# Kernel tuning notes

Hardware: AMD Instinct MI355X
Metric: run time of the kernel (lower is better)

## Reference

```python
import jax, jax.numpy as jnp
import numpy as np

N_NODES = 100000
IN_DIM = 64
OUT_DIM = 64
N_EDGES = 1600000


def _undirected_self_loops(edge_index, num_nodes):
    """Symmetrize, add self loops, coalesce (dedup+sort) like the torch module.
    edge_index is an integer constant, so we preprocess with numpy (no grads flow here).
    Returns (src, dst, w) where w are symmetric GCN normalization weights.
    """
    ei = np.asarray(edge_index, dtype=np.int64)
    loops = np.arange(num_nodes, dtype=np.int64)
    full_src = np.concatenate([ei[0], ei[1], loops])
    full_dst = np.concatenate([ei[1], ei[0], loops])
    keys = np.unique(full_src * num_nodes + full_dst)  # coalesce, sorted
    src = keys // num_nodes
    dst = keys % num_nodes
    deg = np.bincount(dst, minlength=num_nodes).clip(min=1)
    inv_sqrt = deg.astype(np.float32) ** -0.5
    w = inv_sqrt[src] * inv_sqrt[dst]
    return src, dst, w


def setup_inputs() -> dict:
    key = jax.random.key(0)
    kx, kw, kb, ke = jax.random.split(key, 4)
    x = jax.random.normal(kx, (N_NODES, IN_DIM), dtype=jnp.float32)
    # nn.Linear params: W (out, in), b (out,)
    W = jax.random.normal(kw, (OUT_DIM, IN_DIM), dtype=jnp.float32) / np.sqrt(IN_DIM)
    b = jax.random.normal(kb, (OUT_DIM,), dtype=jnp.float32) * 0.01
    edge_index = jax.random.randint(ke, (2, N_EDGES), 0, N_NODES, dtype=jnp.int64)
    return {"x": x, "edge_index": edge_index, "W": W, "b": b}


def reference(x, edge_index, W, b) -> jnp.ndarray:
    n = x.shape[0]
    src_np, dst_np, w_np = _undirected_self_loops(edge_index, n)
    src = jnp.asarray(src_np)
    dst = jnp.asarray(dst_np)
    w = jnp.asarray(w_np).astype(x.dtype)  # (E',)
    h = x @ W.T + b                         # (N, out_dim)
    msg = h[src] * w[:, None]               # gather + per-edge scale, (E', out_dim)
    out = jnp.zeros_like(h).at[dst].add(msg)  # scatter-add aggregation
    return out
```

## Files before the change

kernel.cpp:

```cpp
#include <hip/hip_runtime.h>
#include <hip/hip_bf16.h>
#include <stdint.h>

#define NN 100000
#define EE 1600000
#define CAP 128
#define NB 782
#define CAPB 5120
#define HTS 8192
#define EMPTY 0xFFFFFFFFu
#define BIN_CHUNK 4096
#define GL 782
#define GB ((EE + BIN_CHUNK - 1) / BIN_CHUNK)

__device__ __forceinline__ unsigned int mix32(unsigned int x){
  x ^= x >> 16; x *= 0x7feb352du;
  x ^= x >> 15; x *= 0x846ca68bu;
  x ^= x >> 16;
  return x;
}

extern "C" __global__ __launch_bounds__(256)
void k_prep(const float* __restrict__ x, const float* __restrict__ W,
            const float* __restrict__ bias, __hip_bfloat16* __restrict__ hb,
            const int* __restrict__ ei, int* __restrict__ bcnt,
            unsigned int* __restrict__ bbuf){
  __shared__ __align__(16) char sm[51200];
  const int tid = threadIdx.x;

  if (blockIdx.x < GL){
    float (*wt)[64] = reinterpret_cast<float(*)[64]>(sm);
    float (*xs)[68] = reinterpret_cast<float(*)[68]>(sm + 16384);
    const int lane = tid & 63;
    const int w    = tid >> 6;
    #pragma unroll
    for (int r = 0; r < 16; ++r){
      int i = r*4 + w;
      wt[i][lane] = W[lane*64 + i];
    }
    const int nbase = blockIdx.x * 128;
    #pragma unroll
    for (int r = 0; r < 8; ++r){
      int idx = r*256 + tid;
      int nl  = idx >> 4;
      int c4  = idx & 15;
      int n   = nbase + nl;
      float4 v = make_float4(0.f,0.f,0.f,0.f);
      if (n < NN) v = reinterpret_cast<const float4*>(x)[(size_t)n*16 + c4];
      *reinterpret_cast<float4*>(&xs[nl][c4*4]) = v;
    }
    __syncthreads();

    const int og  = tid & 7;
    const int nl0 = (tid >> 3) * 4;
    float acc[4][8];
    #pragma unroll
    for (int t=0;t<4;++t){
      #pragma unroll
      for (int j=0;j<8;++j) acc[t][j]=0.f;
    }
    #pragma unroll 4
    for (int i=0;i<64;++i){
      float4 wa = *reinterpret_cast<const float4*>(&wt[i][og*8]);
      float4 wb = *reinterpret_cast<const float4*>(&wt[i][og*8+4]);
      #pragma unroll
      for (int t=0;t<4;++t){
        float xv = xs[nl0+t][i];
        acc[t][0] += xv*wa.x; acc[t][1] += xv*wa.y;
        acc[t][2] += xv*wa.z; acc[t][3] += xv*wa.w;
        acc[t][4] += xv*wb.x; acc[t][5] += xv*wb.y;
        acc[t][6] += xv*wb.z; acc[t][7] += xv*wb.w;
      }
    }
    float4 b0 = reinterpret_cast<const float4*>(bias)[og*2];
    float4 b1 = reinterpret_cast<const float4*>(bias)[og*2+1];
    float bb[8] = {b0.x,b0.y,b0.z,b0.w,b1.x,b1.y,b1.z,b1.w};
    #pragma unroll
    for (int t=0;t<4;++t){
      int n = nbase + nl0 + t;
      if (n < NN){
        union { uint4 u4; __hip_bfloat16 v[8]; } pk;
        #pragma unroll
        for (int j=0;j<8;++j) pk.v[j] = __float2bfloat16(acc[t][j] + bb[j]);
        reinterpret_cast<uint4*>(&hb[(size_t)n*64])[og] = pk.u4;
      }
    }
  } else {
    int* hist  = reinterpret_cast<int*>(sm);
    int* bbase = hist + NB;
    int* bcur  = bbase + NB;
    for (int i = tid; i < NB; i += 256) hist[i] = 0;
    __syncthreads();
    const int e0 = (blockIdx.x - GL) * BIN_CHUNK;
    #pragma unroll 1
    for (int r = 0; r < BIN_CHUNK; r += 256){
      int i = e0 + r + tid;
      if (i < EE){
        int a = ei[i], c = ei[EE + i];
        atomicAdd(&hist[c >> 7], 1);
        atomicAdd(&hist[a >> 7], 1);
      }
    }
    __syncthreads();
    for (int bk = tid; bk < NB; bk += 256){
      int hh = hist[bk];
      bbase[bk] = hh ? atomicAdd(&bcnt[bk], hh) : 0;
      bcur[bk]  = 0;
    }
    __syncthreads();
    #pragma unroll 1
    for (int r = 0; r < BIN_CHUNK; r += 256){
      int i = e0 + r + tid;
      if (i < EE){
        int a = ei[i], c = ei[EE + i];
        int b1 = c >> 7, b2 = a >> 7;
        int p1 = bbase[b1] + atomicAdd(&bcur[b1], 1);
        int p2 = bbase[b2] + atomicAdd(&bcur[b2], 1);
        if (p1 < CAPB) bbuf[(size_t)b1*CAPB + p1] = ((unsigned)a << 7) | (unsigned)(c & 127);
        if (p2 < CAPB) bbuf[(size_t)b2*CAPB + p2] = ((unsigned)c << 7) | (unsigned)(a & 127);
      }
    }
  }
}

extern "C" __global__ __launch_bounds__(256)
void k_dedup(const int* __restrict__ bcnt, const unsigned int* __restrict__ bbuf,
             unsigned int* __restrict__ srclist, int* __restrict__ cnt,
             float* __restrict__ inv){
  __shared__ unsigned int HT[HTS];
  __shared__ int dcnt[128], dcur[128];
  const int tid = threadIdx.x;
  const int b   = blockIdx.x;
  const int d0  = b << 7;
  for (int i = tid; i < HTS; i += 256) HT[i] = EMPTY;
  if (tid < 128){ dcnt[tid] = 0; dcur[tid] = 0; }
  __syncthreads();

  int n = bcnt[b]; if (n > CAPB) n = CAPB;
  const unsigned int* buf = bbuf + (size_t)b * CAPB;
  for (int k = tid; k < n; k += 256){
    unsigned int pk  = buf[k];
    unsigned int idx = mix32(pk) & (HTS-1);
    for (;;){
      unsigned int prev = atomicCAS(&HT[idx], EMPTY, pk);
      if (prev == EMPTY || prev == pk) break;
      idx = (idx + 1) & (HTS-1);
    }
  }
  if (tid < 128 && d0 + tid < NN){
    unsigned int pk  = ((unsigned)(d0 + tid) << 7) | (unsigned)tid;
    unsigned int idx = mix32(pk) & (HTS-1);
    for (;;){
      unsigned int prev = atomicCAS(&HT[idx], EMPTY, pk);
      if (prev == EMPTY || prev == pk) break;
      idx = (idx + 1) & (HTS-1);
    }
  }
  __syncthreads();

  for (int i = tid; i < HTS; i += 256){
    unsigned int v = HT[i];
    if (v != EMPTY) atomicAdd(&dcnt[v & 127], 1);
  }
  __syncthreads();
  if (tid < 128 && d0 + tid < NN){
    int c = dcnt[tid];
    cnt[d0 + tid] = c;
    inv[d0 + tid] = rsqrtf((float)c);
  }
  __syncthreads();
  for (int i = tid; i < HTS; i += 256){
    unsigned int v = HT[i];
    if (v != EMPTY){
      int dl  = v & 127;
      int pos = atomicAdd(&dcur[dl], 1);
      if (pos < CAP) srclist[(size_t)(d0 + dl) * CAP + pos] = v >> 7;
    }
  }
}

extern "C" __global__ __launch_bounds__(256)
void k_agg(const __hip_bfloat16* __restrict__ hb, const float* __restrict__ inv,
           const int* __restrict__ cnt, const unsigned int* __restrict__ srclist,
           float* __restrict__ out){
  __shared__ unsigned int ss[4][CAP];
  __shared__ float        sw[4][CAP];
  const int wv   = threadIdx.x >> 6;
  const int lane = threadIdx.x & 63;
  const int d    = blockIdx.x*4 + wv;
  if (d >= NN) return;
  const unsigned int* reg = srclist + (size_t)d * CAP;
  int c = cnt[d]; if (c > CAP) c = CAP;
  const int c8 = (c + 7) & ~7;

  if (lane < c){
    unsigned int s = reg[lane];
    ss[wv][lane] = s;
    sw[wv][lane] = inv[s];
  }
  if (64 + lane < c){
    unsigned int s = reg[64 + lane];
    ss[wv][64 + lane] = s;
    sw[wv][64 + lane] = inv[s];
  }
  {
    int p = c + lane;
    if (p < c8){ ss[wv][p] = 0; sw[wv][p] = 0.f; }
  }
  float acc[8];
  #pragma unroll
  for (int u = 0; u < 8; ++u) acc[u] = 0.f;
  #pragma unroll 1
  for (int j = 0; j < c8; j += 8){
    #pragma unroll
    for (int u = 0; u < 8; ++u){
      unsigned int s = ss[wv][j + u];
      float        w = sw[wv][j + u];
      float       hv = __bfloat162float(hb[(size_t)s * 64 + lane]);
      acc[u] += w * hv;
    }
  }
  float r = ((acc[0]+acc[1]) + (acc[2]+acc[3])) + ((acc[4]+acc[5]) + (acc[6]+acc[7]));
  out[(size_t)d*64 + lane] = r * inv[d];
}

extern "C" void kernel_launch(void* const* d_in, const int* in_sizes, int n_in,
                              void* d_out, int out_size, void* d_ws, size_t ws_size,
                              hipStream_t stream){
  (void)in_sizes; (void)n_in; (void)out_size; (void)ws_size;
  const float* x  = (const float*)d_in[0];
  const int*   ei = (const int*)  d_in[1];
  const float* W  = (const float*)d_in[2];
  const float* b  = (const float*)d_in[3];
  float* out = (float*)d_out;

  char* ws = (char*)d_ws;
  __hip_bfloat16* hb      = (__hip_bfloat16*)ws;
  float*          inv     = (float*)(ws + 12800000);
  int*            cnt     = (int*)  (ws + 13200000);
  unsigned int*   srclist = (unsigned int*)(ws + 13600000);
  int*            bcnt    = (int*)  (ws + 64800000);
  unsigned int*   bbuf    = (unsigned int*)(ws + 64804096);

  hipMemsetAsync(bcnt, 0, NB * 4, stream);

  k_prep  <<<GL + GB, 256, 0, stream>>>(x, W, b, hb, ei, bcnt, bbuf);
  k_dedup <<<NB, 256, 0, stream>>>(bcnt, bbuf, srclist, cnt, inv);
  k_agg   <<<(NN + 3)/4, 256, 0, stream>>>(hb, inv, cnt, srclist, out);
}
```

Baseline: 155.8 us.

## Interleave GEMM and binning blocks, merge dedup count pass, widen agg loads

Three changes at once. The prep kernel now interleaves linear-transform blocks and edge-binning blocks by parity, with a halved binning chunk, so both kinds of work spread evenly across CUs. The dedup kernel drops the separate per-destination counting pass and takes counts from the slot-assignment atomics. The aggregation kernel packs source index and weight into one uint2 in LDS, has each half-wavefront load two bf16 values per 4-byte read over alternating edges, and combines the halves with a shuffle before a float2 store.

```diff
diff --git a/kernel.cpp b/kernel.cpp
--- a/kernel.cpp
+++ b/kernel.cpp
@@ -9,9 +9,9 @@
 #define CAPB 5120
 #define HTS 8192
 #define EMPTY 0xFFFFFFFFu
-#define BIN_CHUNK 4096
+#define BIN_CHUNK 2048
 #define GL 782
-#define GB ((EE + BIN_CHUNK - 1) / BIN_CHUNK)
+#define GB 782
 
 __device__ __forceinline__ unsigned int mix32(unsigned int x){
   x ^= x >> 16; x *= 0x7feb352du;
@@ -28,7 +28,8 @@
   __shared__ __align__(16) char sm[51200];
   const int tid = threadIdx.x;
 
-  if (blockIdx.x < GL){
+  if (!(blockIdx.x & 1)){
+    const int lb = blockIdx.x >> 1;
     float (*wt)[64] = reinterpret_cast<float(*)[64]>(sm);
     float (*xs)[68] = reinterpret_cast<float(*)[68]>(sm + 16384);
     const int lane = tid & 63;
@@ -38,7 +39,7 @@
       int i = r*4 + w;
       wt[i][lane] = W[lane*64 + i];
     }
-    const int nbase = blockIdx.x * 128;
+    const int nbase = lb * 128;
     #pragma unroll
     for (int r = 0; r < 8; ++r){
       int idx = r*256 + tid;
@@ -86,12 +87,13 @@
       }
     }
   } else {
+    const int bb_id = blockIdx.x >> 1;
     int* hist  = reinterpret_cast<int*>(sm);
     int* bbase = hist + NB;
     int* bcur  = bbase + NB;
     for (int i = tid; i < NB; i += 256) hist[i] = 0;
     __syncthreads();
-    const int e0 = (blockIdx.x - GL) * BIN_CHUNK;
+    const int e0 = bb_id * BIN_CHUNK;
     #pragma unroll 1
     for (int r = 0; r < BIN_CHUNK; r += 256){
       int i = e0 + r + tid;
@@ -128,12 +130,12 @@
              unsigned int* __restrict__ srclist, int* __restrict__ cnt,
              float* __restrict__ inv){
   __shared__ unsigned int HT[HTS];
-  __shared__ int dcnt[128], dcur[128];
+  __shared__ int dcur[128];
   const int tid = threadIdx.x;
   const int b   = blockIdx.x;
   const int d0  = b << 7;
   for (int i = tid; i < HTS; i += 256) HT[i] = EMPTY;
-  if (tid < 128){ dcnt[tid] = 0; dcur[tid] = 0; }
+  if (tid < 128) dcur[tid] = 0;
   __syncthreads();
 
   int n = bcnt[b]; if (n > CAPB) n = CAPB;
@@ -160,68 +162,70 @@
 
   for (int i = tid; i < HTS; i += 256){
     unsigned int v = HT[i];
-    if (v != EMPTY) atomicAdd(&dcnt[v & 127], 1);
-  }
-  __syncthreads();
-  if (tid < 128 && d0 + tid < NN){
-    int c = dcnt[tid];
-    cnt[d0 + tid] = c;
-    inv[d0 + tid] = rsqrtf((float)c);
-  }
-  __syncthreads();
-  for (int i = tid; i < HTS; i += 256){
-    unsigned int v = HT[i];
     if (v != EMPTY){
       int dl  = v & 127;
       int pos = atomicAdd(&dcur[dl], 1);
       if (pos < CAP) srclist[(size_t)(d0 + dl) * CAP + pos] = v >> 7;
     }
   }
+  __syncthreads();
+  if (tid < 128 && d0 + tid < NN){
+    int c = dcur[tid];
+    cnt[d0 + tid] = c;
+    inv[d0 + tid] = rsqrtf((float)c);
+  }
 }
 
 extern "C" __global__ __launch_bounds__(256)
 void k_agg(const __hip_bfloat16* __restrict__ hb, const float* __restrict__ inv,
            const int* __restrict__ cnt, const unsigned int* __restrict__ srclist,
            float* __restrict__ out){
-  __shared__ unsigned int ss[4][CAP];
-  __shared__ float        sw[4][CAP];
+  __shared__ uint2 sv[4][CAP];
   const int wv   = threadIdx.x >> 6;
   const int lane = threadIdx.x & 63;
+  const int half = lane >> 5;
+  const int pl   = lane & 31;
   const int d    = blockIdx.x*4 + wv;
   if (d >= NN) return;
   const unsigned int* reg = srclist + (size_t)d * CAP;
   int c = cnt[d]; if (c > CAP) c = CAP;
-  const int c8 = (c + 7) & ~7;
+  const int c16 = (c + 15) & ~15;
 
   if (lane < c){
-    unsigned int s = reg[lane];
-    ss[wv][lane] = s;
-    sw[wv][lane] = inv[s];
+    unsigned s = reg[lane];
+    sv[wv][lane] = make_uint2(s, __float_as_uint(inv[s]));
   }
   if (64 + lane < c){
-    unsigned int s = reg[64 + lane];
-    ss[wv][64 + lane] = s;
-    sw[wv][64 + lane] = inv[s];
-  }
-  {
-    int p = c + lane;
-    if (p < c8){ ss[wv][p] = 0; sw[wv][p] = 0.f; }
-  }
-  float acc[8];
+    unsigned s = reg[64 + lane];
+    sv[wv][64 + lane] = make_uint2(s, __float_as_uint(inv[s]));
+  }
+  { int p = c + lane; if (p < c16) sv[wv][p] = make_uint2(0u, 0u); }
+
+  const char* hbase = (const char*)hb;
+  const int   boff  = pl << 2;
+  float ax[8], ay[8];
   #pragma unroll
-  for (int u = 0; u < 8; ++u) acc[u] = 0.f;
+  for (int u=0;u<8;++u){ ax[u]=0.f; ay[u]=0.f; }
   #pragma unroll 1
-  for (int j = 0; j < c8; j += 8){
+  for (int j = 0; j < c16; j += 16){
     #pragma unroll
     for (int u = 0; u < 8; ++u){
-      unsigned int s = ss[wv][j + u];
-      float        w = sw[wv][j + u];
-      float       hv = __bfloat162float(hb[(size_t)s * 64 + lane]);
-      acc[u] += w * hv;
-    }
-  }
-  float r = ((acc[0]+acc[1]) + (acc[2]+acc[3])) + ((acc[4]+acc[5]) + (acc[6]+acc[7]));
-  out[(size_t)d*64 + lane] = r * inv[d];
+      uint2 e = sv[wv][j + 2*u + half];
+      float w = __uint_as_float(e.y);
+      unsigned hv = *reinterpret_cast<const unsigned*>(hbase + ((size_t)e.x << 7) + boff);
+      ax[u] += w * __uint_as_float(hv << 16);
+      ay[u] += w * __uint_as_float(hv & 0xFFFF0000u);
+    }
+  }
+  float rx = ((ax[0]+ax[1])+(ax[2]+ax[3])) + ((ax[4]+ax[5])+(ax[6]+ax[7]));
+  float ry = ((ay[0]+ay[1])+(ay[2]+ay[3])) + ((ay[4]+ay[5])+(ay[6]+ay[7]));
+  rx += __shfl_xor(rx, 32);
+  ry += __shfl_xor(ry, 32);
+  if (half == 0){
+    float iv = inv[d];
+    float2 o = make_float2(rx * iv, ry * iv);
+    *reinterpret_cast<float2*>(&out[(size_t)d*64 + (pl << 1)]) = o;
+  }
 }
 
 extern "C" void kernel_launch(void* const* d_in, const int* in_sizes, int n_in,
```

Measured after the change: 156.4 us. No clear change (+0.4%).
